# Kernel optimization log

Measured on AMD Instinct MI355X. Metric: run time of the kernel, lower is better.

Reference implementation:

```python
import jax, jax.numpy as jnp
import numpy as np

EMBED = 768
HIDDEN = 768
HEADS = 12
HEAD_DIM = HIDDEN // HEADS


def setup_inputs() -> dict:
    key = jax.random.key(0)
    ks = jax.random.split(key, 9)
    B, S = 16, 512
    lim = 1.0 / np.sqrt(EMBED)
    def lin(kw, kb):
        W = jax.random.uniform(kw, (EMBED, HIDDEN), jnp.float32, -lim, lim)
        b = jax.random.uniform(kb, (HIDDEN,), jnp.float32, -lim, lim)
        return W, b
    Wq, bq = lin(ks[0], ks[1])
    Wk, bk = lin(ks[2], ks[3])
    Wv, bv = lin(ks[4], ks[5])
    inp = jax.random.normal(ks[6], (B, S, EMBED), jnp.float32)
    mask = jax.random.randint(ks[7], (B, S), 0, 2).astype(jnp.float32)
    return {"input": inp, "input_mask": mask,
            "Wq": Wq, "bq": bq, "Wk": Wk, "bk": bk, "Wv": Wv, "bv": bv}


def reference(input, input_mask, Wq, bq, Wk, bk, Wv, bv):
    B, S, _ = input.shape
    # projections -> (B, H, S, D)
    def proj(W, b):
        x = jnp.einsum('bse,eh->bsh', input, W) + b
        return x.reshape(B, S, HEADS, HEAD_DIM).transpose(0, 2, 1, 3)
    Q = proj(Wq, bq)
    K = proj(Wk, bk)
    V = proj(Wv, bv)
    # scores (B, H, S, S), additive mask over keys
    scores = jnp.einsum('bhqd,bhkd->bhqk', Q, K) / jnp.sqrt(jnp.float32(HEAD_DIM))
    bias = (input_mask * -1e9)[:, None, None, :]  # (B,1,1,S) broadcast over heads & queries
    weight = jax.nn.softmax(scores + bias, axis=-1)
    out = jnp.einsum('bhqk,bhkd->bhqd', weight, V)
    return out.transpose(0, 2, 1, 3).reshape(B, S, HIDDEN)
```

## Files before the change

kernel.cpp:

```cpp
#include <hip/hip_runtime.h>
#include <cstdint>
#include <cstddef>

#define B_  16
#define S_  512
#define E_  768
#define NH_ 12
#define D_  64
#define M_  (B_*S_)

typedef unsigned short u16;
typedef __attribute__((ext_vector_type(4))) float f32x4;
typedef __attribute__((ext_vector_type(8))) short bf16x8;

#define LOG2E 1.4426950408889634f

__device__ __forceinline__ u16 f2bf(float f){
  union { float fv; uint32_t u; } v; v.fv = f;
  uint32_t u = v.u;
  uint32_t r = u + 0x7fffu + ((u >> 16) & 1u);
  return (u16)(r >> 16);
}

__global__ __launch_bounds__(256) void cast_x_kernel(const float* __restrict__ x,
                                                     u16* __restrict__ xb, int n4){
  int i = blockIdx.x * 256 + threadIdx.x;
  if (i < n4){
    float4 v = reinterpret_cast<const float4*>(x)[i];
    ushort4 o;
    o.x = f2bf(v.x); o.y = f2bf(v.y); o.z = f2bf(v.z); o.w = f2bf(v.w);
    reinterpret_cast<ushort4*>(xb)[i] = o;
  }
}

__global__ __launch_bounds__(256) void transpose_w_kernel(const float* __restrict__ Wq,
                                                          const float* __restrict__ Wk,
                                                          const float* __restrict__ Wv,
                                                          u16* __restrict__ WtBase){
  __shared__ float t[32][33];
  const float* W = (blockIdx.z == 0) ? Wq : ((blockIdx.z == 1) ? Wk : Wv);
  u16* Wt = WtBase + (size_t)blockIdx.z * E_ * E_;
  int bx = blockIdx.x * 32, by = blockIdx.y * 32;
  int tx = threadIdx.x & 31, ty = threadIdx.x >> 5;
  #pragma unroll
  for (int i = 0; i < 32; i += 8)
    t[ty + i][tx] = W[(size_t)(by + ty + i) * E_ + bx + tx];
  __syncthreads();
  #pragma unroll
  for (int i = 0; i < 32; i += 8)
    Wt[(size_t)(bx + ty + i) * E_ + by + tx] = f2bf(t[tx][ty + i]);
}

__global__ __launch_bounds__(256) void qkv_gemm_kernel(
    const u16* __restrict__ Xb, const u16* __restrict__ WtBase,
    const float* __restrict__ bq, const float* __restrict__ bk, const float* __restrict__ bv,
    u16* __restrict__ Qb, u16* __restrict__ Kb, u16* __restrict__ VtB)
{
  __shared__ u16 lA[8 * 512];
  __shared__ u16 lB[8 * 512];
  const int z = blockIdx.z;
  const u16* Wt = WtBase + (size_t)z * E_ * E_;
  const float* bias = (z == 0) ? bq : ((z == 1) ? bk : bv);
  const int m0 = blockIdx.x * 128;
  const int n0 = blockIdx.y * 128;
  const int tid = threadIdx.x;
  const int lane = tid & 63;
  const int wave = tid >> 6;
  const int wm = wave & 1, wn = wave >> 1;
  const int srow = lane >> 2, skq = lane & 3;
  const int col0 = lane & 15, quad = lane >> 4;

  f32x4 acc[4][4];
  #pragma unroll
  for (int i = 0; i < 4; ++i)
    #pragma unroll
    for (int j = 0; j < 4; ++j)
      acc[i][j] = (f32x4){0.f, 0.f, 0.f, 0.f};

  #pragma unroll 1
  for (int k0 = 0; k0 < E_; k0 += 32){
    __syncthreads();
    #pragma unroll
    for (int cc = 0; cc < 2; ++cc){
      int c = wave * 2 + cc;
      uint4 va = *reinterpret_cast<const uint4*>(Xb + (size_t)(m0 + c*16 + srow) * E_ + k0 + skq*8);
      *reinterpret_cast<uint4*>(&lA[c*512 + (skq*16 + srow)*8]) = va;
      uint4 vb = *reinterpret_cast<const uint4*>(Wt + (size_t)(n0 + c*16 + srow) * E_ + k0 + skq*8);
      *reinterpret_cast<uint4*>(&lB[c*512 + (skq*16 + srow)*8]) = vb;
    }
    __syncthreads();
    bf16x8 af[4], bfr[4];
    #pragma unroll
    for (int mi = 0; mi < 4; ++mi)
      af[mi] = *reinterpret_cast<const bf16x8*>(&lA[(wm*4 + mi)*512 + lane*8]);
    #pragma unroll
    for (int ni = 0; ni < 4; ++ni)
      bfr[ni] = *reinterpret_cast<const bf16x8*>(&lB[(wn*4 + ni)*512 + lane*8]);
    #pragma unroll
    for (int mi = 0; mi < 4; ++mi)
      #pragma unroll
      for (int ni = 0; ni < 4; ++ni)
        acc[mi][ni] = __builtin_amdgcn_mfma_f32_16x16x32_bf16(af[mi], bfr[ni], acc[mi][ni], 0, 0, 0);
  }

  #pragma unroll
  for (int mi = 0; mi < 4; ++mi){
    #pragma unroll
    for (int ni = 0; ni < 4; ++ni){
      int n = n0 + wn*64 + ni*16 + col0;
      float bval = bias[n];
      int h = n >> 6, d = n & 63;
      #pragma unroll
      for (int r = 0; r < 4; ++r){
        int m = m0 + wm*64 + mi*16 + quad*4 + r;
        int b = m >> 9, s = m & 511;
        u16 obf = f2bf(acc[mi][ni][r] + bval);
        size_t bh = (size_t)b * NH_ + h;
        if (z == 0)      Qb[(bh * S_ + s) * D_ + d] = obf;
        else if (z == 1) Kb[(bh * S_ + s) * D_ + d] = obf;
        else             VtB[(bh * D_ + d) * S_ + s] = obf;
      }
    }
  }
}

__global__ __launch_bounds__(256) void attn_kernel(
    const u16* __restrict__ Qb, const u16* __restrict__ Kb, const u16* __restrict__ VtB,
    const float* __restrict__ mask, float* __restrict__ out)
{
  __shared__ u16 lK[8 * 512];
  __shared__ u16 lV[8 * 512];
  __shared__ u16 lP[4 * 1024];
  __shared__ float biasS[S_];
  const int qt = blockIdx.x;
  const int bh = blockIdx.y;
  const int b = bh / NH_, h = bh % NH_;
  const int tid = threadIdx.x, lane = tid & 63, wave = tid >> 6;
  const int col0 = lane & 15, quad = lane >> 4;
  const int srow = lane >> 2, skq = lane & 3;

  for (int i = tid; i < S_; i += 256)
    biasS[i] = mask[b * S_ + i] * -1e9f;

  const int qrow = qt*64 + wave*16 + col0;
  bf16x8 qf[2];
  #pragma unroll
  for (int ks = 0; ks < 2; ++ks)
    qf[ks] = *reinterpret_cast<const bf16x8*>(Qb + ((size_t)bh * S_ + qrow) * D_ + ks*32 + quad*8);

  f32x4 o[4];
  #pragma unroll
  for (int i = 0; i < 4; ++i) o[i] = (f32x4){0.f, 0.f, 0.f, 0.f};
  float mold[4] = {-3.0e38f, -3.0e38f, -3.0e38f, -3.0e38f};
  float lold[4] = {0.f, 0.f, 0.f, 0.f};

  #pragma unroll 1
  for (int st = 0; st < 8; ++st){
    __syncthreads();
    #pragma unroll
    for (int gg = 0; gg < 4; ++gg){
      int g = wave * 4 + gg;
      if (g < 8){
        int ks = g >> 2, nt = g & 3;
        int key = st*64 + nt*16 + srow;
        int d = ks*32 + skq*8;
        uint4 v = *reinterpret_cast<const uint4*>(Kb + ((size_t)bh * S_ + key) * D_ + d);
        *reinterpret_cast<uint4*>(&lK[g*512 + (skq*16 + srow)*8]) = v;
      } else {
        int g2 = g - 8;
        int ks2 = g2 >> 2, nd = g2 & 3;
        int drow = nd*16 + srow;
        int key = st*64 + ks2*32 + skq*8;
        uint4 v = *reinterpret_cast<const uint4*>(VtB + ((size_t)bh * D_ + drow) * S_ + key);
        *reinterpret_cast<uint4*>(&lV[g2*512 + (skq*16 + srow)*8]) = v;
      }
    }
    __syncthreads();

    f32x4 sc[4];
    #pragma unroll
    for (int nt = 0; nt < 4; ++nt) sc[nt] = (f32x4){0.f, 0.f, 0.f, 0.f};
    #pragma unroll
    for (int ks = 0; ks < 2; ++ks){
      #pragma unroll
      for (int nt = 0; nt < 4; ++nt){
        bf16x8 kf = *reinterpret_cast<const bf16x8*>(&lK[(ks*4 + nt)*512 + lane*8]);
        sc[nt] = __builtin_amdgcn_mfma_f32_16x16x32_bf16(qf[ks], kf, sc[nt], 0, 0, 0);
      }
    }
    float vv[4][4];
    #pragma unroll
    for (int nt = 0; nt < 4; ++nt){
      float bb = biasS[st*64 + nt*16 + col0];
      #pragma unroll
      for (int r = 0; r < 4; ++r) vv[nt][r] = sc[nt][r] * 0.125f + bb;
    }
    float mrow[4];
    #pragma unroll
    for (int r = 0; r < 4; ++r)
      mrow[r] = fmaxf(fmaxf(vv[0][r], vv[1][r]), fmaxf(vv[2][r], vv[3][r]));
    #pragma unroll
    for (int off = 1; off <= 8; off <<= 1)
      #pragma unroll
      for (int r = 0; r < 4; ++r)
        mrow[r] = fmaxf(mrow[r], __shfl_xor(mrow[r], off, 64));
    float mnew[4], alpha[4], rsum[4];
    #pragma unroll
    for (int r = 0; r < 4; ++r){
      mnew[r] = fmaxf(mold[r], mrow[r]);
      alpha[r] = exp2f((mold[r] - mnew[r]) * LOG2E);
      rsum[r] = 0.f;
    }
    #pragma unroll
    for (int nt = 0; nt < 4; ++nt){
      int cc = nt*16 + col0;
      int chunkoff = wave*1024 + (nt >> 1)*512;
      int slotbase = ((cc & 31) >> 3) * 16;
      #pragma unroll
      for (int r = 0; r < 4; ++r){
        float p = exp2f((vv[nt][r] - mnew[r]) * LOG2E);
        rsum[r] += p;
        lP[chunkoff + (slotbase + quad*4 + r)*8 + (cc & 7)] = f2bf(p);
      }
    }
    #pragma unroll
    for (int off = 1; off <= 8; off <<= 1)
      #pragma unroll
      for (int r = 0; r < 4; ++r)
        rsum[r] += __shfl_xor(rsum[r], off, 64);
    #pragma unroll
    for (int r = 0; r < 4; ++r){
      lold[r] = alpha[r] * lold[r] + rsum[r];
      mold[r] = mnew[r];
    }
    #pragma unroll
    for (int nd = 0; nd < 4; ++nd)
      #pragma unroll
      for (int r = 0; r < 4; ++r)
        o[nd][r] *= alpha[r];
    bf16x8 pf[2];
    #pragma unroll
    for (int ks2 = 0; ks2 < 2; ++ks2)
      pf[ks2] = *reinterpret_cast<const bf16x8*>(&lP[wave*1024 + ks2*512 + lane*8]);
    #pragma unroll
    for (int ks2 = 0; ks2 < 2; ++ks2){
      #pragma unroll
      for (int nd = 0; nd < 4; ++nd){
        bf16x8 vf = *reinterpret_cast<const bf16x8*>(&lV[(ks2*4 + nd)*512 + lane*8]);
        o[nd] = __builtin_amdgcn_mfma_f32_16x16x32_bf16(pf[ks2], vf, o[nd], 0, 0, 0);
      }
    }
  }

  #pragma unroll
  for (int r = 0; r < 4; ++r){
    int s = qt*64 + wave*16 + quad*4 + r;
    float inv = 1.0f / lold[r];
    #pragma unroll
    for (int nd = 0; nd < 4; ++nd){
      int d = nd*16 + col0;
      out[((size_t)b * S_ + s) * E_ + h*D_ + d] = o[nd][r] * inv;
    }
  }
}

extern "C" void kernel_launch(void* const* d_in, const int* in_sizes, int n_in,
                              void* d_out, int out_size, void* d_ws, size_t ws_size,
                              hipStream_t stream){
  const float* X    = (const float*)d_in[0];
  const float* mask = (const float*)d_in[1];
  const float* Wq   = (const float*)d_in[2];
  const float* bq   = (const float*)d_in[3];
  const float* Wk   = (const float*)d_in[4];
  const float* bk   = (const float*)d_in[5];
  const float* Wv   = (const float*)d_in[6];
  const float* bv   = (const float*)d_in[7];
  float* out = (float*)d_out;

  u16* Xb = (u16*)d_ws;
  u16* Wt = Xb + (size_t)M_ * E_;
  u16* Qb = Wt + (size_t)3 * E_ * E_;
  u16* Kb = Qb + (size_t)M_ * E_;
  u16* Vt = Kb + (size_t)M_ * E_;

  cast_x_kernel<<<(M_ * E_ / 4 + 255) / 256, 256, 0, stream>>>(X, Xb, M_ * E_ / 4);
  transpose_w_kernel<<<dim3(24, 24, 3), 256, 0, stream>>>(Wq, Wk, Wv, Wt);
  qkv_gemm_kernel<<<dim3(64, 6, 3), 256, 0, stream>>>(Xb, Wt, bq, bk, bv, Qb, Kb, Vt);
  attn_kernel<<<dim3(8, 192), 256, 0, stream>>>(Qb, Kb, Vt, mask, out);
}
```

Before: 218.2 us.

## Use global_load_lds DMA and transposed score layout for cheaper softmax

Replaces register-staged global→LDS copies in the QKV GEMM and attention kernels with direct global_load_lds transfers, which frees VGPRs and cuts instruction count. The score MFMA operands are swapped so each lane holds a single query row. Row max and sum then need only two cross-lane shuffles instead of four per row, and P is written to LDS as packed 8-byte stores. Per-row rescale factors are redistributed with shuffles, which adds a few permute ops in exchange.

```diff
diff --git a/kernel.cpp b/kernel.cpp
--- a/kernel.cpp
+++ b/kernel.cpp
@@ -20,6 +20,12 @@
   uint32_t u = v.u;
   uint32_t r = u + 0x7fffu + ((u >> 16) & 1u);
   return (u16)(r >> 16);
+}
+
+__device__ __forceinline__ void gload_lds16(const void* g, void* ldsbase){
+  __builtin_amdgcn_global_load_lds(
+      (const __attribute__((address_space(1))) unsigned int*)g,
+      (__attribute__((address_space(3))) unsigned int*)ldsbase, 16, 0, 0);
 }
 
 __global__ __launch_bounds__(256) void cast_x_kernel(const float* __restrict__ x,
@@ -67,7 +73,8 @@
   const int lane = tid & 63;
   const int wave = tid >> 6;
   const int wm = wave & 1, wn = wave >> 1;
-  const int srow = lane >> 2, skq = lane & 3;
+  const int ls = lane & 15;
+  const int lk = lane >> 4;
   const int col0 = lane & 15, quad = lane >> 4;
 
   f32x4 acc[4][4];
@@ -83,10 +90,8 @@
     #pragma unroll
     for (int cc = 0; cc < 2; ++cc){
       int c = wave * 2 + cc;
-      uint4 va = *reinterpret_cast<const uint4*>(Xb + (size_t)(m0 + c*16 + srow) * E_ + k0 + skq*8);
-      *reinterpret_cast<uint4*>(&lA[c*512 + (skq*16 + srow)*8]) = va;
-      uint4 vb = *reinterpret_cast<const uint4*>(Wt + (size_t)(n0 + c*16 + srow) * E_ + k0 + skq*8);
-      *reinterpret_cast<uint4*>(&lB[c*512 + (skq*16 + srow)*8]) = vb;
+      gload_lds16(Xb + (size_t)(m0 + c*16 + ls) * E_ + k0 + lk*8, &lA[c*512]);
+      gload_lds16(Wt + (size_t)(n0 + c*16 + ls) * E_ + k0 + lk*8, &lB[c*512]);
     }
     __syncthreads();
     bf16x8 af[4], bfr[4];
@@ -137,7 +142,7 @@
   const int b = bh / NH_, h = bh % NH_;
   const int tid = threadIdx.x, lane = tid & 63, wave = tid >> 6;
   const int col0 = lane & 15, quad = lane >> 4;
-  const int srow = lane >> 2, skq = lane & 3;
+  const int ls = lane & 15, lk = lane >> 4;
 
   for (int i = tid; i < S_; i += 256)
     biasS[i] = mask[b * S_ + i] * -1e9f;
@@ -151,8 +156,8 @@
   f32x4 o[4];
   #pragma unroll
   for (int i = 0; i < 4; ++i) o[i] = (f32x4){0.f, 0.f, 0.f, 0.f};
-  float mold[4] = {-3.0e38f, -3.0e38f, -3.0e38f, -3.0e38f};
-  float lold[4] = {0.f, 0.f, 0.f, 0.f};
+  float mold = -3.0e38f;
+  float lold = 0.f;
 
   #pragma unroll 1
   for (int st = 0; st < 8; ++st){
@@ -162,17 +167,13 @@
       int g = wave * 4 + gg;
       if (g < 8){
         int ks = g >> 2, nt = g & 3;
-        int key = st*64 + nt*16 + srow;
-        int d = ks*32 + skq*8;
-        uint4 v = *reinterpret_cast<const uint4*>(Kb + ((size_t)bh * S_ + key) * D_ + d);
-        *reinterpret_cast<uint4*>(&lK[g*512 + (skq*16 + srow)*8]) = v;
+        gload_lds16(Kb + ((size_t)bh * S_ + st*64 + nt*16 + ls) * D_ + ks*32 + lk*8,
+                    &lK[g*512]);
       } else {
         int g2 = g - 8;
         int ks2 = g2 >> 2, nd = g2 & 3;
-        int drow = nd*16 + srow;
-        int key = st*64 + ks2*32 + skq*8;
-        uint4 v = *reinterpret_cast<const uint4*>(VtB + ((size_t)bh * D_ + drow) * S_ + key);
-        *reinterpret_cast<uint4*>(&lV[g2*512 + (skq*16 + srow)*8]) = v;
+        gload_lds16(VtB + ((size_t)bh * D_ + nd*16 + ls) * S_ + st*64 + ks2*32 + lk*8,
+                    &lV[g2*512]);
       }
     }
     __syncthreads();
@@ -185,59 +186,53 @@
       #pragma unroll
       for (int nt = 0; nt < 4; ++nt){
         bf16x8 kf = *reinterpret_cast<const bf16x8*>(&lK[(ks*4 + nt)*512 + lane*8]);
-        sc[nt] = __builtin_amdgcn_mfma_f32_16x16x32_bf16(qf[ks], kf, sc[nt], 0, 0, 0);
+        sc[nt] = __builtin_amdgcn_mfma_f32_16x16x32_bf16(kf, qf[ks], sc[nt], 0, 0, 0);
       }
     }
     float vv[4][4];
     #pragma unroll
     for (int nt = 0; nt < 4; ++nt){
-      float bb = biasS[st*64 + nt*16 + col0];
-      #pragma unroll
-      for (int r = 0; r < 4; ++r) vv[nt][r] = sc[nt][r] * 0.125f + bb;
-    }
-    float mrow[4];
-    #pragma unroll
-    for (int r = 0; r < 4; ++r)
-      mrow[r] = fmaxf(fmaxf(vv[0][r], vv[1][r]), fmaxf(vv[2][r], vv[3][r]));
-    #pragma unroll
-    for (int off = 1; off <= 8; off <<= 1)
+      float4 bb = *reinterpret_cast<const float4*>(&biasS[st*64 + nt*16 + quad*4]);
+      vv[nt][0] = sc[nt][0] * 0.125f + bb.x;
+      vv[nt][1] = sc[nt][1] * 0.125f + bb.y;
+      vv[nt][2] = sc[nt][2] * 0.125f + bb.z;
+      vv[nt][3] = sc[nt][3] * 0.125f + bb.w;
+    }
+    float mrow = vv[0][0];
+    #pragma unroll
+    for (int nt = 0; nt < 4; ++nt)
       #pragma unroll
       for (int r = 0; r < 4; ++r)
-        mrow[r] = fmaxf(mrow[r], __shfl_xor(mrow[r], off, 64));
-    float mnew[4], alpha[4], rsum[4];
+        mrow = fmaxf(mrow, vv[nt][r]);
+    mrow = fmaxf(mrow, __shfl_xor(mrow, 16, 64));
+    mrow = fmaxf(mrow, __shfl_xor(mrow, 32, 64));
+    float mnew = fmaxf(mold, mrow);
+    float alpha = exp2f((mold - mnew) * LOG2E);
+    float rsum = 0.f;
+    #pragma unroll
+    for (int nt = 0; nt < 4; ++nt){
+      ushort4 pw;
+      float p0 = exp2f((vv[nt][0] - mnew) * LOG2E);
+      float p1 = exp2f((vv[nt][1] - mnew) * LOG2E);
+      float p2 = exp2f((vv[nt][2] - mnew) * LOG2E);
+      float p3 = exp2f((vv[nt][3] - mnew) * LOG2E);
+      rsum += (p0 + p1) + (p2 + p3);
+      pw.x = f2bf(p0); pw.y = f2bf(p1); pw.z = f2bf(p2); pw.w = f2bf(p3);
+      int addr = wave*1024 + (nt >> 1)*512
+               + (((nt & 1)*2 + (quad >> 1))*16 + col0)*8 + (quad & 1)*4;
+      *reinterpret_cast<ushort4*>(&lP[addr]) = pw;
+    }
+    rsum += __shfl_xor(rsum, 16, 64);
+    rsum += __shfl_xor(rsum, 32, 64);
+    lold = alpha * lold + rsum;
+    mold = mnew;
     #pragma unroll
     for (int r = 0; r < 4; ++r){
-      mnew[r] = fmaxf(mold[r], mrow[r]);
-      alpha[r] = exp2f((mold[r] - mnew[r]) * LOG2E);
-      rsum[r] = 0.f;
-    }
-    #pragma unroll
-    for (int nt = 0; nt < 4; ++nt){
-      int cc = nt*16 + col0;
-      int chunkoff = wave*1024 + (nt >> 1)*512;
-      int slotbase = ((cc & 31) >> 3) * 16;
-      #pragma unroll
-      for (int r = 0; r < 4; ++r){
-        float p = exp2f((vv[nt][r] - mnew[r]) * LOG2E);
-        rsum[r] += p;
-        lP[chunkoff + (slotbase + quad*4 + r)*8 + (cc & 7)] = f2bf(p);
-      }
-    }
-    #pragma unroll
-    for (int off = 1; off <= 8; off <<= 1)
-      #pragma unroll
-      for (int r = 0; r < 4; ++r)
-        rsum[r] += __shfl_xor(rsum[r], off, 64);
-    #pragma unroll
-    for (int r = 0; r < 4; ++r){
-      lold[r] = alpha[r] * lold[r] + rsum[r];
-      mold[r] = mnew[r];
-    }
-    #pragma unroll
-    for (int nd = 0; nd < 4; ++nd)
-      #pragma unroll
-      for (int r = 0; r < 4; ++r)
-        o[nd][r] *= alpha[r];
+      float ar = __shfl(alpha, (lane & 48) | (quad*4 + r), 64);
+      #pragma unroll
+      for (int nd = 0; nd < 4; ++nd)
+        o[nd][r] *= ar;
+    }
     bf16x8 pf[2];
     #pragma unroll
     for (int ks2 = 0; ks2 < 2; ++ks2)
@@ -255,7 +250,8 @@
   #pragma unroll
   for (int r = 0; r < 4; ++r){
     int s = qt*64 + wave*16 + quad*4 + r;
-    float inv = 1.0f / lold[r];
+    float lr = __shfl(lold, (lane & 48) | (quad*4 + r), 64);
+    float inv = 1.0f / lr;
     #pragma unroll
     for (int nd = 0; nd < 4; ++nd){
       int d = nd*16 + col0;
```

New measurement: 214.4 us. About the same (-1.8%).
